# Performance work log

Measured on AMD Instinct MI355X. Metric: run time of the kernel, lower is better.

The kernel has to match this reference:

```python
import jax, jax.numpy as jnp
import numpy as np

HIDDEN_DIM = 64
EIGS_DIM = 16
N_LAYERS = 2
NUM_USERS = 100000
NUM_ITEMS = 200000
N_NODES = NUM_USERS + NUM_ITEMS
N_EDGES = 1250000
N_PATHS = 14  # 2**(sample_hop+1) - 2 with sample_hop=3
LN_EPS = 1e-5


def setup_inputs() -> dict:
    key = jax.random.key(0)
    k1, k2, k3, k4, k5 = jax.random.split(key, 5)
    return {
        "user_emb": 0.1 * jax.random.normal(k1, (NUM_USERS, HIDDEN_DIM), dtype=jnp.float32),
        "item_emb": 0.1 * jax.random.normal(k2, (NUM_ITEMS, HIDDEN_DIM), dtype=jnp.float32),
        "eigs": jax.random.normal(k3, (N_NODES, EIGS_DIM), dtype=jnp.float32),
        "lambda0": jnp.zeros((N_LAYERS,), dtype=jnp.float32),
        "path_emb_w": jnp.zeros((N_LAYERS, N_PATHS, 1), dtype=jnp.float32),
        "indices": jax.random.randint(k4, (2, N_EDGES), 0, N_NODES, dtype=jnp.int64)
        if jax.config.jax_enable_x64
        else jax.random.randint(k4, (2, N_EDGES), 0, N_NODES, dtype=jnp.int32),
        "path_type": jax.random.randint(k5, (N_EDGES,), 0, N_PATHS, dtype=jnp.int32),
    }


def _layer_norm(x, eps=LN_EPS):
    mu = jnp.mean(x, axis=-1, keepdims=True)
    var = jnp.var(x, axis=-1, keepdims=True)
    return (x - mu) * jax.lax.rsqrt(var + eps)


def _sparse_softmax(row, s, num_nodes):
    # softmax over edges grouped by target-node row index
    m = jax.ops.segment_max(s, row, num_segments=num_nodes)
    e = jnp.exp(s - m[row])
    denom = jax.ops.segment_sum(e, row, num_segments=num_nodes)
    return e / denom[row]


def _attention(y, eigs, row, col, path_type, lam0, pemb):
    sqrt_dim = 1.0 / jnp.sqrt(jnp.float32(HIDDEN_DIM))
    # per-edge q.k score  [E]
    x = jnp.sum(y[row] * y[col], axis=-1) * sqrt_dim
    yeig = jnp.sum(eigs[row] * eigs[col], axis=-1)
    s0 = x + jnp.exp(lam0) * yeig
    s1 = pemb[path_type, 0]
    a0 = _sparse_softmax(row, s0, N_NODES)
    a1 = _sparse_softmax(row, s1, N_NODES)
    a = 0.5 * (a0 + a1)
    # sparse-dense matmul: out[r] = sum_e a_e * v[col_e]
    return jax.ops.segment_sum(a[:, None] * y[col], row, num_segments=N_NODES)


def reference(user_emb, item_emb, eigs, lambda0, path_emb_w, indices, path_type):
    row, col = indices[0], indices[1]
    all_emb = jnp.concatenate([user_emb, item_emb], axis=0)  # [N, d]
    embs = [all_emb]
    for l in range(N_LAYERS):
        y = _layer_norm(all_emb)
        all_emb = _attention(y, eigs, row, col, path_type, lambda0[l], path_emb_w[l])
        embs.append(all_emb)
    light_out = jnp.mean(jnp.stack(embs, axis=1), axis=1)  # [N, d]
    return light_out
```

## Files before the change

### kernel.cpp

```cpp
#include <hip/hip_runtime.h>
#include <hip/hip_bf16.h>

#define HD 64
#define ED 16
#define NU 100000
#define NI 200000
#define NN 300000
#define NE 1250000
#define NP 14

#define RB 512
#define NBKT ((NN + RB - 1) / RB)
#define NR8 (NBKT * RB)
#define BCAP 2432
#define A_ITEMS 16
#define A_CHUNK (256 * A_ITEMS)
#define A_BLOCKS ((NE + A_CHUNK - 1) / A_CHUNK)
#define DBINS 64
#define IT 4

typedef __hip_bfloat16 bf16;
typedef unsigned short ushort8v __attribute__((ext_vector_type(8)));
typedef float  float4v __attribute__((ext_vector_type(4)));
typedef float  float2v __attribute__((ext_vector_type(2)));
typedef int    int2v   __attribute__((ext_vector_type(2)));

__device__ __forceinline__ float bf2f(unsigned short u) {
    union { unsigned int i; float f; } c; c.i = ((unsigned int)u) << 16; return c.f;
}
__device__ __forceinline__ unsigned short f2b(float x) {
    bf16 h = __float2bfloat16(x);
    unsigned short u; __builtin_memcpy(&u, &h, 2); return u;
}

__global__ void ln_kernel(const float* __restrict__ user_emb,
                          const float* __restrict__ item_emb,
                          bf16* __restrict__ yb)
{
    const int tid = blockIdx.x * blockDim.x + threadIdx.x;
    const int r   = tid >> 3;
    const int sub = tid & 7;
    if (r >= NN) return;
    const float* src = (r < NU) ? user_emb + (size_t)r * HD
                                : item_emb + (size_t)(r - NU) * HD;
    const float4 lo = *reinterpret_cast<const float4*>(src + sub * 8);
    const float4 hi = *reinterpret_cast<const float4*>(src + sub * 8 + 4);
    float x[8] = {lo.x, lo.y, lo.z, lo.w, hi.x, hi.y, hi.z, hi.w};

    float sm = 0.0f, sq = 0.0f;
#pragma unroll
    for (int j = 0; j < 8; ++j) { sm += x[j]; sq += x[j] * x[j]; }
    sm += __shfl_xor(sm, 1, 64); sq += __shfl_xor(sq, 1, 64);
    sm += __shfl_xor(sm, 2, 64); sq += __shfl_xor(sq, 2, 64);
    sm += __shfl_xor(sm, 4, 64); sq += __shfl_xor(sq, 4, 64);
    const float mu  = sm * (1.0f / 64.0f);
    const float var = sq * (1.0f / 64.0f) - mu * mu;
    const float inv = rsqrtf(var + 1e-5f);

    ushort8v w;
#pragma unroll
    for (int j = 0; j < 8; ++j) w[j] = f2b((x[j] - mu) * inv);
    *reinterpret_cast<ushort8v*>(yb + (size_t)r * HD + sub * 8) = w;
}

__global__ void bkt_scatter_kernel(const int* __restrict__ row,
                                   const int* __restrict__ col,
                                   const int* __restrict__ pt,
                                   int* __restrict__ wq_bkt,
                                   int* __restrict__ pairs)
{
    __shared__ int hist[NBKT];
    __shared__ int rbase[NBKT];
    __shared__ int roff[NBKT];
    const int tid = threadIdx.x;
    for (int j = tid; j < NBKT; j += 256) { hist[j] = 0; roff[j] = 0; }
    __syncthreads();

    const int base = blockIdx.x * A_CHUNK;
#pragma unroll
    for (int i = 0; i < A_ITEMS; ++i) {
        const int idx = base + i * 256 + tid;
        if (idx < NE) atomicAdd(&hist[row[idx] >> 9], 1);
    }
    __syncthreads();
    for (int j = tid; j < NBKT; j += 256) {
        const int h = hist[j];
        if (h) rbase[j] = atomicAdd(&wq_bkt[j], h);
    }
    __syncthreads();
#pragma unroll
    for (int i = 0; i < A_ITEMS; ++i) {
        const int idx = base + i * 256 + tid;
        if (idx < NE) {
            const int r = row[idx];
            const int b = r >> 9;
            const int v = col[idx] | (pt[idx] << 19) | ((r & (RB - 1)) << 23);
            const int o   = atomicAdd(&roff[b], 1);
            const int rel = rbase[b] + o;
            if (rel < BCAP) pairs[(size_t)b * BCAP + rel] = v;
        }
    }
}

__global__ void bkt_sort_kernel(const int* __restrict__ wq_bkt,
                                const int* __restrict__ pairs,
                                const float* __restrict__ eigs,
                                int2* __restrict__ rinfo,
                                int2* __restrict__ epacked)
{
    __shared__ int rcnt[RB], lrp[RB], wq2[RB], ssum[256];
    __shared__ int dhist[DBINS], dbase[DBINS];
    __shared__ int perml[RB];
    __shared__ float estage[RB * ED];
    const int tid  = threadIdx.x;
    const int b    = blockIdx.x;
    const int r0   = b * RB;
    const int sbase = b * BCAP;
    int cntb = wq_bkt[b]; if (cntb > BCAP) cntb = BCAP;

    for (int j = tid; j < RB; j += 256) { rcnt[j] = 0; wq2[j] = 0; perml[j] = -1; }
    for (int j = tid; j < DBINS; j += 256) dhist[j] = 0;
    for (int k = tid; k < RB * ED; k += 256) {
        const int g = r0 * ED + k;
        estage[k] = (g < NN * ED) ? eigs[g] : 0.0f;
    }
    __syncthreads();

    for (int i = tid; i < cntb; i += 256)
        atomicAdd(&rcnt[(pairs[sbase + i] >> 23) & (RB - 1)], 1);
    __syncthreads();

    const int a0 = rcnt[2 * tid], a1 = rcnt[2 * tid + 1];
    ssum[tid] = a0 + a1;
    __syncthreads();
    for (int off = 1; off < 256; off <<= 1) {
        int x = (tid >= off) ? ssum[tid - off] : 0;
        __syncthreads();
        ssum[tid] += x;
        __syncthreads();
    }
    const int excl = ssum[tid] - (a0 + a1);
    lrp[2 * tid]     = excl;
    lrp[2 * tid + 1] = excl + a0;
    __syncthreads();

    const int ra   = r0 + 2 * tid;
    const int bin0 = (DBINS - 1) - ((a0 < DBINS - 1) ? a0 : (DBINS - 1));
    const int bin1 = (DBINS - 1) - ((a1 < DBINS - 1) ? a1 : (DBINS - 1));
    if (ra < NN)     atomicAdd(&dhist[bin0], 1);
    if (ra + 1 < NN) atomicAdd(&dhist[bin1], 1);
    __syncthreads();
    ssum[tid] = (tid < DBINS) ? dhist[tid] : 0;
    __syncthreads();
    for (int off = 1; off < DBINS; off <<= 1) {
        int x = (tid >= off) ? ssum[tid - off] : 0;
        __syncthreads();
        ssum[tid] += x;
        __syncthreads();
    }
    if (tid < DBINS) { dbase[tid] = ssum[tid] - dhist[tid]; dhist[tid] = 0; }
    __syncthreads();
    if (ra < NN)     perml[dbase[bin0] + atomicAdd(&dhist[bin0], 1)] = 2 * tid;
    if (ra + 1 < NN) perml[dbase[bin1] + atomicAdd(&dhist[bin1], 1)] = 2 * tid + 1;
    __syncthreads();

    for (int j = tid; j < RB; j += 256) {
        const int rl = perml[j];
        int2 out;
        if (rl >= 0) {
            int dg = rcnt[rl]; if (dg > 0xFFF) dg = 0xFFF;
            out = make_int2(sbase + lrp[rl], (r0 + rl) | (dg << 19));
        } else {
            out = make_int2(0, -1);
        }
        rinfo[r0 + j] = out;
    }

    for (int i = tid; i < cntb; i += 256) {
        const int v  = pairs[sbase + i];
        const int rl = (v >> 23) & (RB - 1);
        const int c  = v & 0x7FFFF;
        const float4* ep = reinterpret_cast<const float4*>(eigs + (size_t)c * ED);
        const float4 q0 = ep[0], q1 = ep[1], q2 = ep[2], q3 = ep[3];
        const float* er = estage + rl * ED;
        float d = q0.x * er[0]  + q0.y * er[1]  + q0.z * er[2]  + q0.w * er[3]
                + q1.x * er[4]  + q1.y * er[5]  + q1.z * er[6]  + q1.w * er[7]
                + q2.x * er[8]  + q2.y * er[9]  + q2.z * er[10] + q2.w * er[11]
                + q3.x * er[12] + q3.y * er[13] + q3.z * er[14] + q3.w * er[15];
        const int o   = atomicAdd(&wq2[rl], 1);
        const int pos = sbase + lrp[rl] + o;
        epacked[pos] = make_int2(v & 0x7FFFFF, __float_as_int(d));
    }
}

template <int LAYER>
__global__ __launch_bounds__(256, 4)
void attn_row_kernel(const bf16* __restrict__ yb,
                     const int2* __restrict__ rinfo,
                     const int2* __restrict__ epacked,
                     const float* __restrict__ lambda0,
                     const float* __restrict__ pemb,
                     const float* __restrict__ user_emb,
                     const float* __restrict__ item_emb,
                     bf16* __restrict__ yb_next,
                     float* __restrict__ lntab,
                     float* __restrict__ io)
{
    __shared__ float e1tab[NP];
    if (threadIdx.x < NP)
        e1tab[threadIdx.x] = __expf(pemb[LAYER * NP + threadIdx.x]);
    __syncthreads();

    const int tid  = (int)threadIdx.x;
    const int gl   = tid >> 3;
    const int sub  = tid & 7;
    const int lane = tid & 63;
    const int base = (int)blockIdx.x * (32 * IT);

    const float lam = __expf(lambda0[LAYER]);
    const bf16*  ybs = yb + (size_t)sub * 8;
    const int2v* ep2 = reinterpret_cast<const int2v*>(epacked);

    int2 ri[IT];
#pragma unroll
    for (int it = 0; it < IT; ++it) ri[it] = rinfo[base + it * 32 + gl];

    int2v myv_n;
    {
        const int2v* mp = ep2 + ri[0].x + sub;
        asm volatile("global_load_dwordx2 %0, %1, off" : "=v"(myv_n) : "v"(mp));
        asm volatile("s_waitcnt vmcnt(0)" : "+v"(myv_n));
    }

#pragma unroll
    for (int it = 0; it < IT; ++it) {
        const int2 ric   = ri[it];
        const bool valid = (ric.y >= 0);
        const int r      = valid ? (ric.y & 0x7FFFF) : 0;
        const int deg    = valid ? ((ric.y >> 19) & 0xFFF) : 0;
        const int start  = ric.x;

        int2v myv = myv_n;
        if (sub >= deg) { myv[0] = 0; myv[1] = 0; }

        int   vv[8];
        float ee[8];
#pragma unroll
        for (int kk = 0; kk < 8; ++kk) {
            const int src = (lane & ~7) + kk;
            vv[kk] = __shfl(myv[0], src, 64);
            ee[kk] = __int_as_float(__shfl(myv[1], src, 64));
        }
        const int nb = (deg < 8) ? deg : 8;

        ushort8v yru;
        float4v em_lo = {0,0,0,0}, em_hi = {0,0,0,0};
        float2v ms = {0,0};
        {
            const bf16* yp = ybs + (size_t)r * HD;
            asm volatile("global_load_dwordx4 %0, %1, off" : "=v"(yru) : "v"(yp));
            if (LAYER == 1) {
                const float* ep = ((r < NU) ? user_emb + (size_t)r * HD
                                            : item_emb + (size_t)(r - NU) * HD) + sub * 8;
                asm volatile("global_load_dwordx4 %0, %1, off" : "=v"(em_lo) : "v"(ep));
                asm volatile("global_load_dwordx4 %0, %1, off" : "=v"(em_hi) : "v"(ep + 4));
                const float* tp = lntab + 2 * (size_t)r;
                asm volatile("global_load_dwordx2 %0, %1, off" : "=v"(ms) : "v"(tp));
            }
        }

        const bf16* p0 = ybs + (size_t)(vv[0] & 0x7FFFF) * HD;
        const bf16* p1 = ybs + (size_t)(vv[1] & 0x7FFFF) * HD;
        const bf16* p2 = ybs + (size_t)(vv[2] & 0x7FFFF) * HD;
        const bf16* p3 = ybs + (size_t)(vv[3] & 0x7FFFF) * HD;
        const bf16* p4 = ybs + (size_t)(vv[4] & 0x7FFFF) * HD;
        const bf16* p5 = ybs + (size_t)(vv[5] & 0x7FFFF) * HD;
        const bf16* p6 = ybs + (size_t)(vv[6] & 0x7FFFF) * HD;
        const bf16* p7 = ybs + (size_t)(vv[7] & 0x7FFFF) * HD;
        ushort8v u0, u1, u2, u3, u4, u5, u6, u7;
        asm volatile("global_load_dwordx4 %0, %1, off" : "=v"(u0) : "v"(p0));
        asm volatile("global_load_dwordx4 %0, %1, off" : "=v"(u1) : "v"(p1));
        asm volatile("global_load_dwordx4 %0, %1, off" : "=v"(u2) : "v"(p2));
        asm volatile("global_load_dwordx4 %0, %1, off" : "=v"(u3) : "v"(p3));
        asm volatile("global_load_dwordx4 %0, %1, off" : "=v"(u4) : "v"(p4));
        asm volatile("global_load_dwordx4 %0, %1, off" : "=v"(u5) : "v"(p5));
        asm volatile("global_load_dwordx4 %0, %1, off" : "=v"(u6) : "v"(p6));
        asm volatile("global_load_dwordx4 %0, %1, off" : "=v"(u7) : "v"(p7));

        if (it + 1 < IT) {
            const int2v* mp = ep2 + ri[it + 1].x + sub;
            asm volatile("global_load_dwordx2 %0, %1, off" : "=v"(myv_n) : "v"(mp));
        }

        asm volatile("s_waitcnt vmcnt(0)"
                     : "+v"(u0), "+v"(u1), "+v"(u2), "+v"(u3),
                       "+v"(u4), "+v"(u5), "+v"(u6), "+v"(u7),
                       "+v"(yru), "+v"(em_lo), "+v"(em_hi), "+v"(ms), "+v"(myv_n));

        float yrf[8];
#pragma unroll
        for (int j = 0; j < 8; ++j) yrf[j] = bf2f(yru[j]);

        float U0[8], U1[8];
#pragma unroll
        for (int j = 0; j < 8; ++j) { U0[j] = 0.0f; U1[j] = 0.0f; }
        float d0 = 0.0f, d1 = 0.0f;

        auto consume = [&](const ushort8v& uc, int vk, float ek) {
            float yc[8];
            float sdot = 0.0f;
#pragma unroll
            for (int j = 0; j < 8; ++j) { yc[j] = bf2f(uc[j]); sdot += yrf[j] * yc[j]; }
            sdot += __shfl_xor(sdot, 1, 64);
            sdot += __shfl_xor(sdot, 2, 64);
            sdot += __shfl_xor(sdot, 4, 64);
            const float e0 = __expf(sdot * 0.125f + lam * ek);
            const float e1 = e1tab[(vk >> 19) & 15];
            d0 += e0; d1 += e1;
#pragma unroll
            for (int j = 0; j < 8; ++j) {
                U0[j] += e0 * yc[j];
                U1[j] += e1 * yc[j];
            }
        };
        if (nb > 0) consume(u0, vv[0], ee[0]);
        if (nb > 1) consume(u1, vv[1], ee[1]);
        if (nb > 2) consume(u2, vv[2], ee[2]);
        if (nb > 3) consume(u3, vv[3], ee[3]);
        if (nb > 4) consume(u4, vv[4], ee[4]);
        if (nb > 5) consume(u5, vv[5], ee[5]);
        if (nb > 6) consume(u6, vv[6], ee[6]);
        if (nb > 7) consume(u7, vv[7], ee[7]);

        for (int k0 = 8; k0 < deg; k0 += 8) {
            int2 mv = ((k0 + sub) < deg) ? epacked[start + k0 + sub]
                                         : make_int2(0, 0);
            int   vv2[8];
            float ee2[8];
#pragma unroll
            for (int kk = 0; kk < 8; ++kk) {
                const int src = (lane & ~7) + kk;
                vv2[kk] = __shfl(mv.x, src, 64);
                ee2[kk] = __int_as_float(__shfl(mv.y, src, 64));
            }
            const int nb2 = ((deg - k0) < 8) ? (deg - k0) : 8;
#pragma unroll
            for (int kk = 0; kk < 8; ++kk) {
                if (kk < nb2) {
                    ushort8v uc = *reinterpret_cast<const ushort8v*>(
                        ybs + (size_t)(vv2[kk] & 0x7FFFF) * HD);
                    consume(uc, vv2[kk], ee2[kk]);
                }
            }
        }

        const float i0 = deg ? 0.5f / d0 : 0.0f;
        const float i1 = deg ? 0.5f / d1 : 0.0f;
        float acc[8];
#pragma unroll
        for (int j = 0; j < 8; ++j) acc[j] = i0 * U0[j] + i1 * U1[j];

        if (LAYER == 0) {
            if (valid) {
                float sm = 0.0f, sq = 0.0f;
#pragma unroll
                for (int j = 0; j < 8; ++j) { sm += acc[j]; sq += acc[j] * acc[j]; }
                sm += __shfl_xor(sm, 1, 64); sq += __shfl_xor(sq, 1, 64);
                sm += __shfl_xor(sm, 2, 64); sq += __shfl_xor(sq, 2, 64);
                sm += __shfl_xor(sm, 4, 64); sq += __shfl_xor(sq, 4, 64);
                const float mu  = sm * (1.0f / 64.0f);
                const float var = sq * (1.0f / 64.0f) - mu * mu;
                const float inv = rsqrtf(var + 1e-5f);
                ushort8v w;
#pragma unroll
                for (int j = 0; j < 8; ++j) w[j] = f2b((acc[j] - mu) * inv);
                *reinterpret_cast<ushort8v*>(yb_next + (size_t)r * HD + sub * 8) = w;
                if (sub == 0) {
                    float2v t; t[0] = mu; t[1] = sqrtf(var + 1e-5f);
                    *reinterpret_cast<float2v*>(lntab + 2 * (size_t)r) = t;
                }
            }
        } else {
            if (valid) {
                float* iorow = io + (size_t)r * HD + sub * 8;
                const float third = 1.0f / 3.0f;
                float4v o0, o1;
#pragma unroll
                for (int j = 0; j < 4; ++j) {
                    const float out1 = yrf[j] * ms[1] + ms[0];
                    o0[j] = (em_lo[j] + out1 + acc[j]) * third;
                }
#pragma unroll
                for (int j = 0; j < 4; ++j) {
                    const float out1 = yrf[j + 4] * ms[1] + ms[0];
                    o1[j] = (em_hi[j] + out1 + acc[j + 4]) * third;
                }
                *reinterpret_cast<float4v*>(iorow)     = o0;
                *reinterpret_cast<float4v*>(iorow + 4) = o1;
            }
        }
    }
}

extern "C" void kernel_launch(void* const* d_in, const int* in_sizes, int n_in,
                              void* d_out, int out_size, void* d_ws, size_t ws_size,
                              hipStream_t stream)
{
    const float* user_emb = (const float*)d_in[0];
    const float* item_emb = (const float*)d_in[1];
    const float* eigs     = (const float*)d_in[2];
    const float* lambda0  = (const float*)d_in[3];
    const float* pemb     = (const float*)d_in[4];
    const int*   indices  = (const int*)d_in[5];
    const int*   ptype    = (const int*)d_in[6];
    const int*   row = indices;
    const int*   col = indices + NE;

    float* io = (float*)d_out;
    char*  ws = (char*)d_ws;
    bf16*  yb      = (bf16*)ws;
    bf16*  yb2     = yb + (size_t)NN * HD;
    int*   pairs   = (int*)(yb2 + (size_t)NN * HD);
    int2*  epacked = (int2*)(pairs + (size_t)NBKT * BCAP);
    int2*  rinfo   = epacked + (size_t)NBKT * BCAP;
    float* lntab   = (float*)(rinfo + NR8);
    int*   wq_bkt  = (int*)(lntab + 2 * (size_t)NN);

    const dim3 blk(256);
    const int gridAttn = NR8 / (32 * IT);

    ln_kernel<<<(NN * 8 + 255) / 256, blk, 0, stream>>>(user_emb, item_emb, yb);

    hipMemsetAsync(wq_bkt, 0, NBKT * sizeof(int), stream);
    bkt_scatter_kernel<<<A_BLOCKS, blk, 0, stream>>>(row, col, ptype, wq_bkt, pairs);
    bkt_sort_kernel<<<NBKT, blk, 0, stream>>>(wq_bkt, pairs, eigs, rinfo, epacked);

    attn_row_kernel<0><<<gridAttn, blk, 0, stream>>>(yb, rinfo, epacked,
                                                     lambda0, pemb, user_emb,
                                                     item_emb, yb2, lntab, io);
    attn_row_kernel<1><<<gridAttn, blk, 0, stream>>>(yb2, rinfo, epacked,
                                                     lambda0, pemb, user_emb,
                                                     item_emb, nullptr, lntab, io);
}
```

Before: 376.5 us.

## Widen bucket sort to 512 threads, permute row order, halve scatter chunk

```diff
diff --git a/kernel.cpp b/kernel.cpp
--- a/kernel.cpp
+++ b/kernel.cpp
@@ -13,7 +13,7 @@
 #define NBKT ((NN + RB - 1) / RB)
 #define NR8 (NBKT * RB)
 #define BCAP 2432
-#define A_ITEMS 16
+#define A_ITEMS 8
 #define A_CHUNK (256 * A_ITEMS)
 #define A_BLOCKS ((NE + A_CHUNK - 1) / A_CHUNK)
 #define DBINS 64
@@ -102,13 +102,14 @@
     }
 }
 
-__global__ void bkt_sort_kernel(const int* __restrict__ wq_bkt,
-                                const int* __restrict__ pairs,
-                                const float* __restrict__ eigs,
-                                int2* __restrict__ rinfo,
-                                int2* __restrict__ epacked)
+__global__ __launch_bounds__(512)
+void bkt_sort_kernel(const int* __restrict__ wq_bkt,
+                     const int* __restrict__ pairs,
+                     const float* __restrict__ eigs,
+                     int2* __restrict__ rinfo,
+                     int2* __restrict__ epacked)
 {
-    __shared__ int rcnt[RB], lrp[RB], wq2[RB], ssum[256];
+    __shared__ int rcnt[RB], lrp[RB], wq2[RB], ssum[RB];
     __shared__ int dhist[DBINS], dbase[DBINS];
     __shared__ int perml[RB];
     __shared__ float estage[RB * ED];
@@ -118,53 +119,52 @@
     const int sbase = b * BCAP;
     int cntb = wq_bkt[b]; if (cntb > BCAP) cntb = BCAP;
 
-    for (int j = tid; j < RB; j += 256) { rcnt[j] = 0; wq2[j] = 0; perml[j] = -1; }
-    for (int j = tid; j < DBINS; j += 256) dhist[j] = 0;
-    for (int k = tid; k < RB * ED; k += 256) {
+    rcnt[tid] = 0; wq2[tid] = 0; perml[tid] = -1;
+    if (tid < DBINS) dhist[tid] = 0;
+    for (int k = tid; k < RB * ED; k += 512) {
         const int g = r0 * ED + k;
         estage[k] = (g < NN * ED) ? eigs[g] : 0.0f;
     }
     __syncthreads();
 
-    for (int i = tid; i < cntb; i += 256)
+    for (int i = tid; i < cntb; i += 512)
         atomicAdd(&rcnt[(pairs[sbase + i] >> 23) & (RB - 1)], 1);
     __syncthreads();
 
-    const int a0 = rcnt[2 * tid], a1 = rcnt[2 * tid + 1];
-    ssum[tid] = a0 + a1;
-    __syncthreads();
-    for (int off = 1; off < 256; off <<= 1) {
+    const int myc = rcnt[tid];
+    ssum[tid] = myc;
+    __syncthreads();
+    for (int off = 1; off < RB; off <<= 1) {
         int x = (tid >= off) ? ssum[tid - off] : 0;
         __syncthreads();
         ssum[tid] += x;
         __syncthreads();
     }
-    const int excl = ssum[tid] - (a0 + a1);
-    lrp[2 * tid]     = excl;
-    lrp[2 * tid + 1] = excl + a0;
-    __syncthreads();
-
-    const int ra   = r0 + 2 * tid;
-    const int bin0 = (DBINS - 1) - ((a0 < DBINS - 1) ? a0 : (DBINS - 1));
-    const int bin1 = (DBINS - 1) - ((a1 < DBINS - 1) ? a1 : (DBINS - 1));
-    if (ra < NN)     atomicAdd(&dhist[bin0], 1);
-    if (ra + 1 < NN) atomicAdd(&dhist[bin1], 1);
-    __syncthreads();
-    ssum[tid] = (tid < DBINS) ? dhist[tid] : 0;
+    lrp[tid] = ssum[tid] - myc;
+    __syncthreads();
+
+    const int ra  = r0 + tid;
+    const int bin = (DBINS - 1) - ((myc < DBINS - 1) ? myc : (DBINS - 1));
+    if (ra < NN) atomicAdd(&dhist[bin], 1);
+    __syncthreads();
+    if (tid < DBINS) ssum[tid] = dhist[tid];
     __syncthreads();
     for (int off = 1; off < DBINS; off <<= 1) {
-        int x = (tid >= off) ? ssum[tid - off] : 0;
+        int x = (tid < DBINS && tid >= off) ? ssum[tid - off] : 0;
         __syncthreads();
-        ssum[tid] += x;
+        if (tid < DBINS) ssum[tid] += x;
         __syncthreads();
     }
     if (tid < DBINS) { dbase[tid] = ssum[tid] - dhist[tid]; dhist[tid] = 0; }
     __syncthreads();
-    if (ra < NN)     perml[dbase[bin0] + atomicAdd(&dhist[bin0], 1)] = 2 * tid;
-    if (ra + 1 < NN) perml[dbase[bin1] + atomicAdd(&dhist[bin1], 1)] = 2 * tid + 1;
-    __syncthreads();
-
-    for (int j = tid; j < RB; j += 256) {
+    if (ra < NN) perml[dbase[bin] + atomicAdd(&dhist[bin], 1)] = tid;
+    __syncthreads();
+
+    {
+        const int j  = tid;
+        const int R  = j >> 3, o = j & 7;
+        const int N  = ((R & 3) << 4) | (R >> 2);
+        const int pos = (N << 3) | o;
         const int rl = perml[j];
         int2 out;
         if (rl >= 0) {
@@ -173,10 +173,10 @@
         } else {
             out = make_int2(0, -1);
         }
-        rinfo[r0 + j] = out;
-    }
-
-    for (int i = tid; i < cntb; i += 256) {
+        rinfo[r0 + pos] = out;
+    }
+
+    for (int i = tid; i < cntb; i += 512) {
         const int v  = pairs[sbase + i];
         const int rl = (v >> 23) & (RB - 1);
         const int c  = v & 0x7FFFF;
@@ -433,7 +433,7 @@
 
     hipMemsetAsync(wq_bkt, 0, NBKT * sizeof(int), stream);
     bkt_scatter_kernel<<<A_BLOCKS, blk, 0, stream>>>(row, col, ptype, wq_bkt, pairs);
-    bkt_sort_kernel<<<NBKT, blk, 0, stream>>>(wq_bkt, pairs, eigs, rinfo, epacked);
+    bkt_sort_kernel<<<NBKT, dim3(512), 0, stream>>>(wq_bkt, pairs, eigs, rinfo, epacked);
 
     attn_row_kernel<0><<<gridAttn, blk, 0, stream>>>(yb, rinfo, epacked,
                                                      lambda0, pemb, user_emb,
```

Result: faster. 355.3 us (-5.6%).
